# Kernel tuning notes

Measured on AMD Instinct MI355X. Metric: run time of the kernel, lower is better.

The kernel has to match this reference:

```python
import jax, jax.numpy as jnp
import numpy as np

HEADS = 8
DIM_HEAD = 64
SCALE = DIM_HEAD ** -0.5


def setup_inputs() -> dict:
    key = jax.random.key(0)
    k1, k2, k3 = jax.random.split(key, 3)
    B, N, D = 4, 2048, 512
    inner = HEADS * DIM_HEAD  # 512
    x = jax.random.normal(k1, (B, N, D), dtype=jnp.float32)
    # nn.Linear stores weight [out, in]; y = x @ W.T
    w_qkv = jax.random.normal(k2, (3 * inner, D), dtype=jnp.float32) * (D ** -0.5)
    w_out = jax.random.normal(k3, (D, inner), dtype=jnp.float32) * (inner ** -0.5)
    b_out = jnp.zeros((D,), dtype=jnp.float32)
    return {"x": x, "w_qkv": w_qkv, "w_out": w_out, "b_out": b_out}


def reference(x, w_qkv, w_out, b_out):
    B, N, D = x.shape
    qkv = jnp.einsum('bnd,ed->bne', x, w_qkv)  # [B,N,3*inner]
    q, k, v = jnp.split(qkv, 3, axis=-1)
    def to_heads(t):
        return t.reshape(B, N, HEADS, DIM_HEAD).transpose(0, 2, 1, 3)  # [B,H,N,Dh]
    q, k, v = to_heads(q), to_heads(k), to_heads(v)
    dots = jnp.einsum('bhid,bhjd->bhij', q, k) * SCALE  # [B,H,N,N]
    attn = jax.nn.softmax(dots, axis=-1)
    out = jnp.einsum('bhij,bhjd->bhid', attn, v)  # [B,H,N,Dh]
    out = out.transpose(0, 2, 1, 3).reshape(B, N, HEADS * DIM_HEAD)
    return jnp.einsum('bne,de->bnd', out, w_out) + b_out
```

## Files before the change

### kernel.cpp

```cpp
#include <hip/hip_runtime.h>
#include <hip/hip_bf16.h>
#include <stdint.h>

typedef __bf16 bf16;
typedef __bf16 bf16x8 __attribute__((ext_vector_type(8)));
typedef __bf16 bf16x4 __attribute__((ext_vector_type(4)));
typedef float f32x4 __attribute__((ext_vector_type(4)));

template <int V> struct Int { static constexpr int value = V; };

static __device__ __forceinline__ void gl2lds16(const void* g, void* l) {
  const __attribute__((address_space(1))) void* gp =
      reinterpret_cast<const __attribute__((address_space(1))) void*>(
          reinterpret_cast<uintptr_t>(g));
  __attribute__((address_space(3))) void* lp =
      reinterpret_cast<__attribute__((address_space(3))) void*>(
          static_cast<uint32_t>(reinterpret_cast<uintptr_t>(l)));
  __builtin_amdgcn_global_load_lds(gp, lp, 16, 0, 0);
}

static __device__ __forceinline__ float fast_exp2(float x) {
#if __has_builtin(__builtin_amdgcn_exp2f)
  return __builtin_amdgcn_exp2f(x);
#else
  return exp2f(x);
#endif
}

__global__ __launch_bounds__(256) void cvt_f32_bf16(const float* __restrict__ src,
                                                    bf16* __restrict__ dst, int n4) {
  int i = blockIdx.x * blockDim.x + threadIdx.x;
  const int stride = gridDim.x * blockDim.x;
  for (; i < n4; i += stride) {
    const float4 v = reinterpret_cast<const float4*>(src)[i];
    bf16x4 o;
    o[0] = (bf16)v.x; o[1] = (bf16)v.y; o[2] = (bf16)v.z; o[3] = (bf16)v.w;
    reinterpret_cast<bf16x4*>(dst)[i] = o;
  }
}

__global__ __launch_bounds__(256) void qkv_gemm(const bf16* __restrict__ X,
                                                const bf16* __restrict__ W,
                                                bf16* __restrict__ Qb,
                                                bf16* __restrict__ Kb,
                                                bf16* __restrict__ Vt) {
  __shared__ __align__(16) bf16 AshX[8192];
  __shared__ __align__(16) bf16 BshX[8192];
  const int t = threadIdx.x;
  const int lane = t & 63;
  const int w = t >> 6;
  const int fr = lane & 15, fg = lane >> 4;
  const int wr = w >> 1, wc = w & 1;
  const int m0 = blockIdx.x * 128;
  const int n0 = blockIdx.y * 128;
  const int r0 = t >> 2, seg = t & 3;
  const bf16* pA0 = X + (m0 + r0) * 512 + seg * 8;
  const bf16* pA1 = X + (m0 + r0 + 64) * 512 + seg * 8;
  const bf16* pB0 = W + (n0 + r0) * 512 + seg * 8;
  const bf16* pB1 = W + (n0 + r0 + 64) * 512 + seg * 8;
  const bf16* ap = AshX + (wr * 64 + fr) * 32 + fg * 8;
  const bf16* bp = BshX + (wc * 64 + fr) * 32 + fg * 8;

  f32x4 acc[4][4] = {};

  auto stage = [&](auto Bt) {
    constexpr int B = decltype(Bt)::value;
    gl2lds16(pA0, (void*)(AshX + B * 4096 + t * 8));
    gl2lds16(pA1, (void*)(AshX + B * 4096 + 2048 + t * 8));
    gl2lds16(pB0, (void*)(BshX + B * 4096 + t * 8));
    gl2lds16(pB1, (void*)(BshX + B * 4096 + 2048 + t * 8));
    pA0 += 32; pA1 += 32; pB0 += 32; pB1 += 32;
  };
  auto step = [&](auto Bt) {
    constexpr int B = decltype(Bt)::value;
    bf16x8 a[4], b[4];
#pragma unroll
    for (int m = 0; m < 4; ++m) a[m] = *reinterpret_cast<const bf16x8*>(ap + B * 4096 + m * 512);
#pragma unroll
    for (int n = 0; n < 4; ++n) b[n] = *reinterpret_cast<const bf16x8*>(bp + B * 4096 + n * 512);
#pragma unroll
    for (int m = 0; m < 4; ++m)
#pragma unroll
      for (int n = 0; n < 4; ++n)
        acc[m][n] = __builtin_amdgcn_mfma_f32_16x16x32_bf16(a[m], b[n], acc[m][n], 0, 0, 0);
  };

  stage(Int<0>{});
  __syncthreads();
  for (int kt = 0; kt < 16; kt += 2) {
    stage(Int<1>{});
    step(Int<0>{});
    __syncthreads();
    if (kt < 14) stage(Int<0>{});
    step(Int<1>{});
    __syncthreads();
  }

  const int which = n0 >> 9;
#pragma unroll
  for (int n = 0; n < 4; ++n) {
    const int e = n0 + wc * 64 + 16 * n + fr;
    const int h = (e >> 6) & 7;
    const int d = e & 63;
#pragma unroll
    for (int m = 0; m < 4; ++m) {
      const int mbase = m0 + wr * 64 + 16 * m + fg * 4;
      if (which == 2) {
        bf16x4 pk;
#pragma unroll
        for (int r = 0; r < 4; ++r) pk[r] = (bf16)acc[m][n][r];
        const int b = mbase >> 11, tok = mbase & 2047;
        *reinterpret_cast<bf16x4*>(&Vt[((b * 8 + h) * 64 + d) * 2048 + tok]) = pk;
      } else {
        bf16* dst = (which == 0) ? Qb : Kb;
        const float sc = (which == 0) ? (0.125f * 1.44269504088896f) : 1.0f;
#pragma unroll
        for (int r = 0; r < 4; ++r) {
          const int row = mbase + r;
          const int b = row >> 11, tok = row & 2047;
          dst[((b * 8 + h) * 2048 + tok) * 64 + d] = (bf16)(acc[m][n][r] * sc);
        }
      }
    }
  }
}

__global__ __launch_bounds__(256, 4) void attn_fwd(const bf16* __restrict__ Qb,
                                                   const bf16* __restrict__ Kb,
                                                   const bf16* __restrict__ Vt,
                                                   bf16* __restrict__ Ob) {
  __shared__ __align__(16) bf16 sh[16384];
  const int t = threadIdx.x;
  const int lane = t & 63;
  const int w = t >> 6;
  const int fr = lane & 15, fg = lane >> 4;
  const int bh = blockIdx.x;
  const int q0 = blockIdx.y * 64 + 16 * w;

  const bf16* Qrow = Qb + (bh * 2048 + q0 + fr) * 64;
  const bf16x8 qf0 = *reinterpret_cast<const bf16x8*>(Qrow + fg * 8);
  const bf16x8 qf1 = *reinterpret_cast<const bf16x8*>(Qrow + 32 + fg * 8);

  bf16x8 ones;
#pragma unroll
  for (int i = 0; i < 8; ++i) ones[i] = (bf16)1.0f;

  const int c0row = t >> 3, cseg = t & 7;
  const int c1row = c0row + 32;
  const int s0 = (cseg ^ (c0row & 7)) * 8;
  const int s1 = (cseg ^ (c1row & 7)) * 8;
  const int kp0 = 32 * ((c0row >> 4) >> 1) + 8 * ((c0row & 15) >> 2) +
                  4 * ((c0row >> 4) & 1) + (c0row & 3);
  const int kp1 = 32 * ((c1row >> 4) >> 1) + 8 * ((c1row & 15) >> 2) +
                  4 * ((c1row >> 4) & 1) + (c1row & 3);
  const bf16* pK0 = Kb + bh * 131072 + kp0 * 64 + s0;
  const bf16* pK1 = Kb + bh * 131072 + kp1 * 64 + s1;
  const bf16* pV0 = Vt + bh * 131072 + c0row * 2048 + s0;
  const bf16* pV1 = Vt + bh * 131072 + c1row * 2048 + s1;

  const int swz = (fr & 7) << 4;
  const int ko0 = fr * 128 + ((fg * 16) ^ swz);
  const int ko1 = fr * 128 + ((64 + fg * 16) ^ swz);
  const char* shb = reinterpret_cast<const char*>(sh);

  f32x4 oacc[4] = {};
  f32x4 lacc = {};

  auto stage = [&](auto Bt) {
    constexpr int B = decltype(Bt)::value;
    gl2lds16(pK0, (void*)(sh + B * 4096 + t * 8));
    gl2lds16(pK1, (void*)(sh + B * 4096 + 2048 + t * 8));
    gl2lds16(pV0, (void*)(sh + 8192 + B * 4096 + t * 8));
    gl2lds16(pV1, (void*)(sh + 8192 + B * 4096 + 2048 + t * 8));
    pK0 += 4096; pK1 += 4096; pV0 += 64; pV1 += 64;
  };

  auto compute = [&](auto Bt) {
    constexpr int B = decltype(Bt)::value;
    f32x4 s[4] = {};
#pragma unroll
    for (int j = 0; j < 4; ++j) {
      const bf16x8 kf0 = *reinterpret_cast<const bf16x8*>(shb + ko0 + (B * 8192 + j * 2048));
      s[j] = __builtin_amdgcn_mfma_f32_16x16x32_bf16(kf0, qf0, s[j], 0, 0, 0);
      const bf16x8 kf1 = *reinterpret_cast<const bf16x8*>(shb + ko1 + (B * 8192 + j * 2048));
      s[j] = __builtin_amdgcn_mfma_f32_16x16x32_bf16(kf1, qf1, s[j], 0, 0, 0);
    }
    bf16x8 pf[2];
#pragma unroll
    for (int j = 0; j < 4; ++j)
#pragma unroll
      for (int r = 0; r < 4; ++r) {
        pf[j >> 1][4 * (j & 1) + r] = (bf16)fast_exp2(s[j][r]);
      }
    __builtin_amdgcn_s_setprio(1);
#pragma unroll
    for (int ss = 0; ss < 2; ++ss) {
      lacc = __builtin_amdgcn_mfma_f32_16x16x32_bf16(ones, pf[ss], lacc, 0, 0, 0);
#pragma unroll
      for (int j = 0; j < 4; ++j) {
        const bf16x8 vf = *reinterpret_cast<const bf16x8*>(
            shb + (ss ? ko1 : ko0) + (16384 + B * 8192 + j * 2048));
        oacc[j] = __builtin_amdgcn_mfma_f32_16x16x32_bf16(vf, pf[ss], oacc[j], 0, 0, 0);
      }
    }
    __builtin_amdgcn_s_setprio(0);
  };

  stage(Int<0>{});
  __syncthreads();
  for (int kt = 0; kt < 32; kt += 2) {
    stage(Int<1>{});
    compute(Int<0>{});
    __syncthreads();
    if (kt < 30) stage(Int<0>{});
    compute(Int<1>{});
    __syncthreads();
  }

  const int b = bh >> 3, h = bh & 7;
  const int q = q0 + fr;
  const float inv = 1.0f / lacc[0];
#pragma unroll
  for (int j = 0; j < 4; ++j) {
    bf16x4 o4;
#pragma unroll
    for (int r = 0; r < 4; ++r) o4[r] = (bf16)(oacc[j][r] * inv);
    *reinterpret_cast<bf16x4*>(&Ob[(b * 2048 + q) * 512 + h * 64 + 16 * j + 4 * fg]) = o4;
  }
}

__global__ __launch_bounds__(256) void out_gemm(const bf16* __restrict__ O,
                                                const bf16* __restrict__ W,
                                                const float* __restrict__ bias,
                                                float* __restrict__ Y) {
  __shared__ __align__(16) bf16 Ash[2][64 * 32];
  __shared__ __align__(16) bf16 Bsh[2][64 * 32];
  const int t = threadIdx.x;
  const int lane = t & 63;
  const int w = t >> 6;
  const int fr = lane & 15, fg = lane >> 4;
  const int m0 = blockIdx.x * 64;
  const int n0 = blockIdx.y * 64;
  const int srow = t >> 2, sseg = t & 3;
  const bf16* gA = O + (m0 + srow) * 512 + sseg * 8;
  const bf16* gB = W + (n0 + srow) * 512 + sseg * 8;

  f32x4 acc[4] = {};
  gl2lds16(gA, &Ash[0][t * 8]);
  gl2lds16(gB, &Bsh[0][t * 8]);
  __syncthreads();
  int cur = 0;
  for (int kt = 0; kt < 16; ++kt) {
    if (kt < 15) {
      gl2lds16(gA + (kt + 1) * 32, &Ash[cur ^ 1][t * 8]);
      gl2lds16(gB + (kt + 1) * 32, &Bsh[cur ^ 1][t * 8]);
    }
    const bf16x8 a = *reinterpret_cast<const bf16x8*>(&Ash[cur][(16 * w + fr) * 32 + fg * 8]);
#pragma unroll
    for (int j = 0; j < 4; ++j) {
      const bf16x8 b = *reinterpret_cast<const bf16x8*>(&Bsh[cur][(16 * j + fr) * 32 + fg * 8]);
      acc[j] = __builtin_amdgcn_mfma_f32_16x16x32_bf16(a, b, acc[j], 0, 0, 0);
    }
    __syncthreads();
    cur ^= 1;
  }
  const int mbase = m0 + 16 * w + fg * 4;
#pragma unroll
  for (int j = 0; j < 4; ++j) {
    const int col = n0 + 16 * j + fr;
    const float bv = bias[col];
#pragma unroll
    for (int r = 0; r < 4; ++r) {
      Y[(mbase + r) * 512 + col] = acc[j][r] + bv;
    }
  }
}

extern "C" void kernel_launch(void* const* d_in, const int* in_sizes, int n_in,
                              void* d_out, int out_size, void* d_ws, size_t ws_size,
                              hipStream_t stream) {
  const float* x = (const float*)d_in[0];
  const float* w_qkv = (const float*)d_in[1];
  const float* w_out = (const float*)d_in[2];
  const float* b_out = (const float*)d_in[3];
  float* y = (float*)d_out;
  char* ws = (char*)d_ws;
  bf16* xb    = (bf16*)(ws);
  bf16* wqkvb = (bf16*)(ws + 8388608);
  bf16* woutb = (bf16*)(ws + 9961472);
  bf16* Qb    = (bf16*)(ws + 10485760);
  bf16* Kb    = (bf16*)(ws + 18874368);
  bf16* Vt    = (bf16*)(ws + 27262976);
  bf16* Ob    = (bf16*)(ws + 35651584);

  hipLaunchKernelGGL(cvt_f32_bf16, dim3(2048), dim3(256), 0, stream, x, xb, 4194304 / 4);
  hipLaunchKernelGGL(cvt_f32_bf16, dim3(768), dim3(256), 0, stream, w_qkv, wqkvb, 786432 / 4);
  hipLaunchKernelGGL(cvt_f32_bf16, dim3(256), dim3(256), 0, stream, w_out, woutb, 262144 / 4);
  hipLaunchKernelGGL(qkv_gemm, dim3(64, 12), dim3(256), 0, stream, xb, wqkvb, Qb, Kb, Vt);
  hipLaunchKernelGGL(attn_fwd, dim3(32, 32), dim3(256), 0, stream, Qb, Kb, Vt, Ob);
  hipLaunchKernelGGL(out_gemm, dim3(128, 8), dim3(256), 0, stream, Ob, woutb, b_out, y);
}
```

Baseline: 86.94 us.

## Deepen attention K/V pipeline to four stages and fuse conversion kernels

The attention kernel now uses a four-stage LDS ring buffer with explicit vmcnt waits and a single barrier per tile, replacing the double-buffer with two syncthreads per tile. LDS doubles to 64KB and launch bounds drop to two blocks per SM, trading occupancy for deeper prefetch. The grid mapping is swapped so consecutive blocks share the same head's K/V, which may improve L2 reuse. The three fp32-to-bf16 conversion launches are merged into one kernel, relying on the workspace buffers being contiguous. The first QK MFMA also takes a zero accumulator instead of a zero-initialised array.

```diff
diff --git a/kernel.cpp b/kernel.cpp
--- a/kernel.cpp
+++ b/kernel.cpp
@@ -27,12 +27,16 @@
 #endif
 }
 
-__global__ __launch_bounds__(256) void cvt_f32_bf16(const float* __restrict__ src,
-                                                    bf16* __restrict__ dst, int n4) {
-  int i = blockIdx.x * blockDim.x + threadIdx.x;
-  const int stride = gridDim.x * blockDim.x;
-  for (; i < n4; i += stride) {
-    const float4 v = reinterpret_cast<const float4*>(src)[i];
+__global__ __launch_bounds__(256) void cvt_all(const float* __restrict__ x,
+                                               const float* __restrict__ wq,
+                                               const float* __restrict__ wo,
+                                               bf16* __restrict__ dst) {
+  int i = blockIdx.x * 256 + threadIdx.x;
+  const int stride = gridDim.x * 256;
+  for (; i < 1310720; i += stride) {
+    const float4 v = (i < 1048576) ? reinterpret_cast<const float4*>(x)[i]
+                   : (i < 1245184) ? reinterpret_cast<const float4*>(wq)[i - 1048576]
+                                   : reinterpret_cast<const float4*>(wo)[i - 1245184];
     bf16x4 o;
     o[0] = (bf16)v.x; o[1] = (bf16)v.y; o[2] = (bf16)v.z; o[3] = (bf16)v.w;
     reinterpret_cast<bf16x4*>(dst)[i] = o;
@@ -125,17 +129,17 @@
   }
 }
 
-__global__ __launch_bounds__(256, 4) void attn_fwd(const bf16* __restrict__ Qb,
+__global__ __launch_bounds__(256, 2) void attn_fwd(const bf16* __restrict__ Qb,
                                                    const bf16* __restrict__ Kb,
                                                    const bf16* __restrict__ Vt,
                                                    bf16* __restrict__ Ob) {
-  __shared__ __align__(16) bf16 sh[16384];
+  __shared__ __align__(16) bf16 sh[32768];
   const int t = threadIdx.x;
   const int lane = t & 63;
   const int w = t >> 6;
   const int fr = lane & 15, fg = lane >> 4;
-  const int bh = blockIdx.x;
-  const int q0 = blockIdx.y * 64 + 16 * w;
+  const int bh = blockIdx.y;
+  const int q0 = blockIdx.x * 64 + 16 * w;
 
   const bf16* Qrow = Qb + (bh * 2048 + q0 + fr) * 64;
   const bf16x8 qf0 = *reinterpret_cast<const bf16x8*>(Qrow + fg * 8);
@@ -165,24 +169,25 @@
 
   f32x4 oacc[4] = {};
   f32x4 lacc = {};
-
-  auto stage = [&](auto Bt) {
-    constexpr int B = decltype(Bt)::value;
-    gl2lds16(pK0, (void*)(sh + B * 4096 + t * 8));
-    gl2lds16(pK1, (void*)(sh + B * 4096 + 2048 + t * 8));
-    gl2lds16(pV0, (void*)(sh + 8192 + B * 4096 + t * 8));
-    gl2lds16(pV1, (void*)(sh + 8192 + B * 4096 + 2048 + t * 8));
+  const f32x4 fzero = {0.f, 0.f, 0.f, 0.f};
+
+  auto stage = [&](auto St) {
+    constexpr int S = decltype(St)::value;
+    gl2lds16(pK0, (void*)(sh + S * 4096 + t * 8));
+    gl2lds16(pK1, (void*)(sh + S * 4096 + 2048 + t * 8));
+    gl2lds16(pV0, (void*)(sh + 16384 + S * 4096 + t * 8));
+    gl2lds16(pV1, (void*)(sh + 16384 + S * 4096 + 2048 + t * 8));
     pK0 += 4096; pK1 += 4096; pV0 += 64; pV1 += 64;
   };
 
-  auto compute = [&](auto Bt) {
-    constexpr int B = decltype(Bt)::value;
-    f32x4 s[4] = {};
+  auto compute = [&](auto St) {
+    constexpr int S = decltype(St)::value;
+    f32x4 s[4];
 #pragma unroll
     for (int j = 0; j < 4; ++j) {
-      const bf16x8 kf0 = *reinterpret_cast<const bf16x8*>(shb + ko0 + (B * 8192 + j * 2048));
-      s[j] = __builtin_amdgcn_mfma_f32_16x16x32_bf16(kf0, qf0, s[j], 0, 0, 0);
-      const bf16x8 kf1 = *reinterpret_cast<const bf16x8*>(shb + ko1 + (B * 8192 + j * 2048));
+      const bf16x8 kf0 = *reinterpret_cast<const bf16x8*>(shb + ko0 + (S * 8192 + j * 2048));
+      s[j] = __builtin_amdgcn_mfma_f32_16x16x32_bf16(kf0, qf0, fzero, 0, 0, 0);
+      const bf16x8 kf1 = *reinterpret_cast<const bf16x8*>(shb + ko1 + (S * 8192 + j * 2048));
       s[j] = __builtin_amdgcn_mfma_f32_16x16x32_bf16(kf1, qf1, s[j], 0, 0, 0);
     }
     bf16x8 pf[2];
@@ -199,23 +204,37 @@
 #pragma unroll
       for (int j = 0; j < 4; ++j) {
         const bf16x8 vf = *reinterpret_cast<const bf16x8*>(
-            shb + (ss ? ko1 : ko0) + (16384 + B * 8192 + j * 2048));
+            shb + (ss ? ko1 : ko0) + (32768 + S * 8192 + j * 2048));
         oacc[j] = __builtin_amdgcn_mfma_f32_16x16x32_bf16(vf, pf[ss], oacc[j], 0, 0, 0);
       }
     }
     __builtin_amdgcn_s_setprio(0);
   };
 
+  auto phase = [&](auto ReadS, auto StageS, auto Vm) {
+    constexpr int ST = decltype(StageS)::value;
+    constexpr int VM = decltype(Vm)::value;
+    if constexpr (ST >= 0) stage(Int<ST>{});
+    if constexpr (VM == 8) asm volatile("s_waitcnt vmcnt(8)" ::: "memory");
+    else if constexpr (VM == 4) asm volatile("s_waitcnt vmcnt(4)" ::: "memory");
+    else asm volatile("s_waitcnt vmcnt(0)" ::: "memory");
+    __builtin_amdgcn_s_barrier();
+    __builtin_amdgcn_sched_barrier(0);
+    compute(ReadS);
+  };
+
   stage(Int<0>{});
-  __syncthreads();
-  for (int kt = 0; kt < 32; kt += 2) {
-    stage(Int<1>{});
-    compute(Int<0>{});
-    __syncthreads();
-    if (kt < 30) stage(Int<0>{});
-    compute(Int<1>{});
-    __syncthreads();
-  }
+  stage(Int<1>{});
+  for (int kt = 0; kt < 28; kt += 4) {
+    phase(Int<0>{}, Int<2>{}, Int<8>{});
+    phase(Int<1>{}, Int<3>{}, Int<8>{});
+    phase(Int<2>{}, Int<0>{}, Int<8>{});
+    phase(Int<3>{}, Int<1>{}, Int<8>{});
+  }
+  phase(Int<0>{}, Int<2>{}, Int<8>{});
+  phase(Int<1>{}, Int<3>{}, Int<8>{});
+  phase(Int<2>{}, Int<-1>{}, Int<4>{});
+  phase(Int<3>{}, Int<-1>{}, Int<0>{});
 
   const int b = bh >> 3, h = bh & 7;
   const int q = q0 + fr;
@@ -293,9 +312,7 @@
   bf16* Vt    = (bf16*)(ws + 27262976);
   bf16* Ob    = (bf16*)(ws + 35651584);
 
-  hipLaunchKernelGGL(cvt_f32_bf16, dim3(2048), dim3(256), 0, stream, x, xb, 4194304 / 4);
-  hipLaunchKernelGGL(cvt_f32_bf16, dim3(768), dim3(256), 0, stream, w_qkv, wqkvb, 786432 / 4);
-  hipLaunchKernelGGL(cvt_f32_bf16, dim3(256), dim3(256), 0, stream, w_out, woutb, 262144 / 4);
+  hipLaunchKernelGGL(cvt_all, dim3(5120), dim3(256), 0, stream, x, w_qkv, w_out, xb);
   hipLaunchKernelGGL(qkv_gemm, dim3(64, 12), dim3(256), 0, stream, xb, wqkvb, Qb, Kb, Vt);
   hipLaunchKernelGGL(attn_fwd, dim3(32, 32), dim3(256), 0, stream, Qb, Kb, Vt, Ob);
   hipLaunchKernelGGL(out_gemm, dim3(128, 8), dim3(256), 0, stream, Ob, woutb, b_out, y);
```

New measurement: 84.76 us. -2.5%, faster.
